# Kernel optimization log

Hardware: AMD Instinct MI355X
Metric: run time of the kernel (lower is better)

The kernel has to match this reference:

```python
import jax, jax.numpy as jnp
import numpy as np

B, S, E, H = 4, 1024, 1024, 16
D = E // H          # head_dim = 64
F = 4 * E           # mlp inner = 4096
EPS = 1e-5


def _layernorm(x, scale, bias):
    mu = jnp.mean(x, axis=-1, keepdims=True)
    var = jnp.var(x, axis=-1, keepdims=True)
    return (x - mu) * jax.lax.rsqrt(var + EPS) * scale + bias


def setup_inputs() -> dict:
    key = jax.random.key(0)
    ks = jax.random.split(key, 8)
    std = 0.02
    return {
        "hidden_states": jax.random.normal(ks[0], (B, S, E), jnp.float32),
        "ln1_scale": jnp.ones((E,), jnp.float32),
        "ln1_bias": jnp.zeros((E,), jnp.float32),
        # Conv1D kernels stored as (out_features, in_features), applied as x @ k.T
        "w_attn": jax.random.normal(ks[1], (3 * E, E), jnp.float32) * std,
        "b_attn": jnp.zeros((3 * E,), jnp.float32),
        "w_proj": jax.random.normal(ks[2], (E, E), jnp.float32) * std,
        "b_proj": jnp.zeros((E,), jnp.float32),
        "ln2_scale": jnp.ones((E,), jnp.float32),
        "ln2_bias": jnp.zeros((E,), jnp.float32),
        "w_fc": jax.random.normal(ks[3], (F, E), jnp.float32) * std,
        "b_fc": jnp.zeros((F,), jnp.float32),
        "w_proj2": jax.random.normal(ks[4], (E, F), jnp.float32) * std,
        "b_proj2": jnp.zeros((E,), jnp.float32),
    }


def reference(hidden_states, ln1_scale, ln1_bias, w_attn, b_attn, w_proj, b_proj,
              ln2_scale, ln2_bias, w_fc, b_fc, w_proj2, b_proj2):
    x = hidden_states
    # --- attention sub-block ---
    h = _layernorm(x, ln1_scale, ln1_bias)
    qkv = h @ w_attn.T + b_attn                      # [B,S,3E]
    q, k, v = jnp.split(qkv, 3, axis=2)
    q = q.reshape(B, S, H, D) / jnp.sqrt(jnp.float32(D))
    k = k.reshape(B, S, H, D)
    v = v.reshape(B, S, H, D)
    # NOTE: source sets attention_bias = None, so NO causal mask is applied.
    logits = jnp.einsum("bqhd,bkhd->bhqk", q, k)     # [B,H,S,S]
    attn = jax.nn.softmax(logits, axis=-1)
    o = jnp.einsum("bhqk,bkhd->bqhd", attn, v).reshape(B, S, E)
    o = o @ w_proj.T + b_proj
    x = x + o
    # --- mlp sub-block ---
    h = _layernorm(x, ln2_scale, ln2_bias)
    m = jax.nn.gelu(h @ w_fc.T + b_fc, approximate=True)  # gelu_new
    m = m @ w_proj2.T + b_proj2
    return x + m
```

## Files before the change

kernel.cpp:

```cpp
#include <hip/hip_runtime.h>

#define DEV __device__ __forceinline__

using bf16x8 = __attribute__((ext_vector_type(8))) __bf16;
using f32x4  = __attribute__((ext_vector_type(4))) float;
typedef unsigned int u32;
typedef unsigned short u16;
typedef unsigned long long u64;

static constexpr int Bb = 4, Ss = 1024, Ee = 1024, Hh = 16, Dd = 64, Ff = 4096;
static constexpr int Mm = Bb * Ss;

DEV u16 f2bf(float f) {
  union { float f; u32 u; } v; v.f = f;
  u32 r = v.u + 0x7fffu + ((v.u >> 16) & 1u);
  return (u16)(r >> 16);
}

DEV void gload16(const void* g, void* lds) {
  __builtin_amdgcn_global_load_lds(
      (const __attribute__((address_space(1))) void*)(u64)g,
      (__attribute__((address_space(3))) void*)(u32)(u64)lds,
      16, 0, 0);
}

DEV float gelu_tanh(float x) {
  float x3 = x * x * x;
  float t  = tanhf(0.7978845608028654f * (x + 0.044715f * x3));
  return 0.5f * x * (1.0f + t);
}

DEV int swz(int row, int col) { return row * 64 + (col ^ ((row & 7) << 3)); }

__global__ __launch_bounds__(256) void cvt_bf16(const float* __restrict__ in,
                                                u16* __restrict__ out, int n) {
  int i = (blockIdx.x * 256 + threadIdx.x) * 8;
  if (i >= n) return;
  float4 a = *(const float4*)(in + i);
  float4 b = *(const float4*)(in + i + 4);
  uint4 o;
  o.x = (u32)f2bf(a.x) | ((u32)f2bf(a.y) << 16);
  o.y = (u32)f2bf(a.z) | ((u32)f2bf(a.w) << 16);
  o.z = (u32)f2bf(b.x) | ((u32)f2bf(b.y) << 16);
  o.w = (u32)f2bf(b.z) | ((u32)f2bf(b.w) << 16);
  *(uint4*)(out + i) = o;
}

__global__ __launch_bounds__(256) void ln_kernel(const float* __restrict__ x,
                                                 const float* __restrict__ scale,
                                                 const float* __restrict__ bias,
                                                 u16* __restrict__ h) {
  const int row = blockIdx.x, tid = threadIdx.x;
  const float4 v = ((const float4*)(x + (size_t)row * Ee))[tid];
  float s  = v.x + v.y + v.z + v.w;
  float ss = v.x * v.x + v.y * v.y + v.z * v.z + v.w * v.w;
  for (int m = 1; m < 64; m <<= 1) {
    s  += __shfl_xor(s, m, 64);
    ss += __shfl_xor(ss, m, 64);
  }
  __shared__ float red[8];
  const int w = tid >> 6, ln = tid & 63;
  if (ln == 0) { red[w * 2] = s; red[w * 2 + 1] = ss; }
  __syncthreads();
  s  = red[0] + red[2] + red[4] + red[6];
  ss = red[1] + red[3] + red[5] + red[7];
  const float mu   = s * (1.0f / Ee);
  const float var  = ss * (1.0f / Ee) - mu * mu;
  const float rstd = rsqrtf(var + 1e-5f);
  const float4 sc = ((const float4*)scale)[tid];
  const float4 bi = ((const float4*)bias)[tid];
  ushort4 o;
  o.x = f2bf((v.x - mu) * rstd * sc.x + bi.x);
  o.y = f2bf((v.y - mu) * rstd * sc.y + bi.y);
  o.z = f2bf((v.z - mu) * rstd * sc.z + bi.z);
  o.w = f2bf((v.w - mu) * rstd * sc.w + bi.w);
  ((ushort4*)(h + (size_t)row * Ee))[tid] = o;
}

template <int EPI>
__global__ __launch_bounds__(256, 3) void gemm2(
    const u16* __restrict__ A, const u16* __restrict__ Bw,
    const float* __restrict__ bias, const float* __restrict__ resid,
    float* __restrict__ outf, u16* __restrict__ outb,
    u16* __restrict__ q, u16* __restrict__ k, u16* __restrict__ v,
    int N, int K) {
  __shared__ u16 As[3][128 * 32];
  __shared__ u16 Bs[3][128 * 32];
  const int tid = threadIdx.x;
  const int w = tid >> 6, ln = tid & 63;
  const int lr = ln & 15, lg = ln >> 4;

  const int nwg = gridDim.x * gridDim.y;
  const int bid = blockIdx.y * gridDim.x + blockIdx.x;
  const int sid = (bid & 7) * (nwg >> 3) + (bid >> 3);
  const int bx = sid % gridDim.x, by = sid / gridDim.x;
  const int tm = by * 128, tn = bx * 128;
  const int wr = (w >> 1) * 64, wc = (w & 1) * 64;

  f32x4 zero4 = {0.f, 0.f, 0.f, 0.f};
  f32x4 acc[4][4];
#pragma unroll
  for (int i = 0; i < 4; ++i)
#pragma unroll
    for (int j = 0; j < 4; ++j) acc[i][j] = zero4;

  const int r0 = tid >> 2, sl = tid & 3;
  const int cs = (sl ^ (r0 & 3)) * 8;
  const u16* aP0 = A  + (size_t)(tm + r0) * K + cs;
  const u16* aP1 = A  + (size_t)(tm + 64 + r0) * K + cs;
  const u16* bP0 = Bw + (size_t)(tn + r0) * K + cs;
  const u16* bP1 = Bw + (size_t)(tn + 64 + r0) * K + cs;

  auto STAGE = [&](int buf, int k0) {
    gload16(aP0 + k0, &As[buf][tid * 8]);
    gload16(aP1 + k0, &As[buf][(256 + tid) * 8]);
    gload16(bP0 + k0, &Bs[buf][tid * 8]);
    gload16(bP1 + k0, &Bs[buf][(256 + tid) * 8]);
  };

  const int nt = K >> 5;
  STAGE(0, 0);
  STAGE(1, 32);
  asm volatile("s_waitcnt vmcnt(4)" ::: "memory");
  __builtin_amdgcn_s_barrier();
  __builtin_amdgcn_sched_barrier(0);

  for (int t = 0; t < nt; ++t) {
    const int cur = t % 3;
    const bool more = (t + 2) < nt;
    if (more) STAGE((t + 2) % 3, (t + 2) << 5);

    bf16x8 af[4], bb[4];
#pragma unroll
    for (int mi = 0; mi < 4; ++mi) {
      const int row = wr + mi * 16 + lr;
      af[mi] = *(const bf16x8*)&As[cur][row * 32 + ((lg ^ (row & 3)) << 3)];
    }
#pragma unroll
    for (int ni = 0; ni < 4; ++ni) {
      const int row = wc + ni * 16 + lr;
      bb[ni] = *(const bf16x8*)&Bs[cur][row * 32 + ((lg ^ (row & 3)) << 3)];
    }
    __builtin_amdgcn_s_setprio(1);
#pragma unroll
    for (int mi = 0; mi < 4; ++mi)
#pragma unroll
      for (int ni = 0; ni < 4; ++ni)
        acc[mi][ni] = __builtin_amdgcn_mfma_f32_16x16x32_bf16(
            af[mi], bb[ni], acc[mi][ni], 0, 0, 0);
    __builtin_amdgcn_s_setprio(0);
    __builtin_amdgcn_sched_barrier(0);
    if (more) asm volatile("s_waitcnt vmcnt(4)" ::: "memory");
    else      asm volatile("s_waitcnt vmcnt(0)" ::: "memory");
    __builtin_amdgcn_s_barrier();
    __builtin_amdgcn_sched_barrier(0);
  }

#pragma unroll
  for (int mi = 0; mi < 4; ++mi) {
#pragma unroll
    for (int ni = 0; ni < 4; ++ni) {
      const int gc = tn + wc + ni * 16 + lr;
#pragma unroll
      for (int j = 0; j < 4; ++j) {
        const int gr = tm + wr + mi * 16 + lg * 4 + j;
        float val = acc[mi][ni][j] + bias[gc];
        if constexpr (EPI == 0) {
          const int which = gc >> 10, hh = (gc >> 6) & 15, dd = gc & 63;
          const int bb2 = gr >> 10, ss2 = gr & 1023;
          const size_t dst = ((size_t)(bb2 * 16 + hh) * 1024 + ss2) * 64 + dd;
          if (which == 0)      q[dst] = f2bf(val * 0.125f);
          else if (which == 1) k[dst] = f2bf(val);
          else                 v[dst] = f2bf(val);
        } else if constexpr (EPI == 1) {
          const size_t idx = (size_t)gr * N + gc;
          outf[idx] = val + resid[idx];
        } else {
          outb[(size_t)gr * N + gc] = f2bf(gelu_tanh(val));
        }
      }
    }
  }
}

__global__ __launch_bounds__(256) void attn_kernel(const u16* __restrict__ qg,
                                                   const u16* __restrict__ kg,
                                                   const u16* __restrict__ vg,
                                                   u16* __restrict__ ao) {
  __shared__ u16 Qs[64 * 64], Ks[64 * 64], Vt[64 * 64], Ps[64 * 64];
  const int tid = threadIdx.x;
  const int w = tid >> 6, ln = tid & 63;
  const int lr = ln & 15, lg = ln >> 4;
  const int bh = blockIdx.y;
  const int q0 = blockIdx.x * 64;
  const size_t head = (size_t)bh * (Ss * Dd);

  {
    const u16* src = qg + head + (size_t)q0 * Dd;
#pragma unroll
    for (int i = 0; i < 2; ++i) {
      const int gi = i * 256 + tid, row = gi >> 3, g = gi & 7;
      *(uint4*)&Qs[row * 64 + ((g ^ (row & 7)) << 3)] = *(const uint4*)(src + gi * 8);
    }
  }

  f32x4 zero4 = {0.f, 0.f, 0.f, 0.f};
  f32x4 acc_o[4] = {zero4, zero4, zero4, zero4};
  float mrow[4] = {-1e30f, -1e30f, -1e30f, -1e30f};
  float lrow[4] = {0.f, 0.f, 0.f, 0.f};

  for (int kt = 0; kt < 16; ++kt) {
    __syncthreads();
    const u16* ksrc = kg + head + (size_t)kt * 64 * Dd;
    const u16* vsrc = vg + head + (size_t)kt * 64 * Dd;
#pragma unroll
    for (int i = 0; i < 2; ++i) {
      const int gi = i * 256 + tid, row = gi >> 3, g = gi & 7;
      *(uint4*)&Ks[row * 64 + ((g ^ (row & 7)) << 3)] = *(const uint4*)(ksrc + gi * 8);
    }
#pragma unroll
    for (int i = 0; i < 2; ++i) {
      const int kv = i * 32 + (tid >> 3), d0 = (tid & 7) * 8;
      uint4 dv = *(const uint4*)(vsrc + (size_t)kv * Dd + d0);
      const u16* pv = (const u16*)&dv;
#pragma unroll
      for (int j = 0; j < 8; ++j) {
        const int dd = d0 + j;
        Vt[dd * 64 + (((kv >> 3) ^ (dd & 7)) << 3) + (kv & 7)] = pv[j];
      }
    }
    __syncthreads();

    bf16x8 aq[2];
#pragma unroll
    for (int kk = 0; kk < 2; ++kk)
      aq[kk] = *(const bf16x8*)&Qs[swz(w * 16 + lr, kk * 32 + lg * 8)];
    f32x4 sa[4];
#pragma unroll
    for (int kf = 0; kf < 4; ++kf) {
      f32x4 s = zero4;
#pragma unroll
      for (int kk = 0; kk < 2; ++kk) {
        bf16x8 bk = *(const bf16x8*)&Ks[swz(kf * 16 + lr, kk * 32 + lg * 8)];
        s = __builtin_amdgcn_mfma_f32_16x16x32_bf16(aq[kk], bk, s, 0, 0, 0);
      }
      sa[kf] = s;
    }

#pragma unroll
    for (int j = 0; j < 4; ++j) {
      float mx = fmaxf(fmaxf(sa[0][j], sa[1][j]), fmaxf(sa[2][j], sa[3][j]));
      mx = fmaxf(mx, __shfl_xor(mx, 1, 64));
      mx = fmaxf(mx, __shfl_xor(mx, 2, 64));
      mx = fmaxf(mx, __shfl_xor(mx, 4, 64));
      mx = fmaxf(mx, __shfl_xor(mx, 8, 64));
      const float nm = fmaxf(mrow[j], mx);
      const float corr = __expf(mrow[j] - nm);
      mrow[j] = nm;
      float ssum = 0.f;
#pragma unroll
      for (int kf = 0; kf < 4; ++kf) {
        const float p = __expf(sa[kf][j] - nm);
        sa[kf][j] = p;
        ssum += p;
      }
      ssum += __shfl_xor(ssum, 1, 64);
      ssum += __shfl_xor(ssum, 2, 64);
      ssum += __shfl_xor(ssum, 4, 64);
      ssum += __shfl_xor(ssum, 8, 64);
      lrow[j] = lrow[j] * corr + ssum;
#pragma unroll
      for (int df = 0; df < 4; ++df) acc_o[df][j] *= corr;
    }

#pragma unroll
    for (int kf = 0; kf < 4; ++kf)
#pragma unroll
      for (int j = 0; j < 4; ++j)
        Ps[swz(w * 16 + lg * 4 + j, kf * 16 + lr)] = f2bf(sa[kf][j]);

    __syncthreads();

    bf16x8 ap[2];
#pragma unroll
    for (int kk = 0; kk < 2; ++kk)
      ap[kk] = *(const bf16x8*)&Ps[swz(w * 16 + lr, kk * 32 + lg * 8)];
#pragma unroll
    for (int df = 0; df < 4; ++df) {
#pragma unroll
      for (int kk = 0; kk < 2; ++kk) {
        bf16x8 bv = *(const bf16x8*)&Vt[swz(df * 16 + lr, kk * 32 + lg * 8)];
        acc_o[df] = __builtin_amdgcn_mfma_f32_16x16x32_bf16(ap[kk], bv, acc_o[df], 0, 0, 0);
      }
    }
  }

  const int b = bh >> 4, h = bh & 15;
#pragma unroll
  for (int df = 0; df < 4; ++df) {
#pragma unroll
    for (int j = 0; j < 4; ++j) {
      const int srow = q0 + w * 16 + lg * 4 + j;
      const int e = h * 64 + df * 16 + lr;
      ao[((size_t)b * Ss + srow) * Ee + e] = f2bf(acc_o[df][j] / lrow[j]);
    }
  }
}

extern "C" void kernel_launch(void* const* d_in, const int* in_sizes, int n_in,
                              void* d_out, int out_size, void* d_ws, size_t ws_size,
                              hipStream_t stream) {
  const float* x      = (const float*)d_in[0];
  const float* ln1_s  = (const float*)d_in[1];
  const float* ln1_b  = (const float*)d_in[2];
  const float* w_attn = (const float*)d_in[3];
  const float* b_attn = (const float*)d_in[4];
  const float* w_proj = (const float*)d_in[5];
  const float* b_proj = (const float*)d_in[6];
  const float* ln2_s  = (const float*)d_in[7];
  const float* ln2_b  = (const float*)d_in[8];
  const float* w_fc   = (const float*)d_in[9];
  const float* b_fc   = (const float*)d_in[10];
  const float* w_proj2= (const float*)d_in[11];
  const float* b_proj2= (const float*)d_in[12];
  float* out = (float*)d_out;

  char* base = (char*)d_ws;
  size_t off = 0;
  auto alloc = [&](size_t bytes) { char* p = base + off; off += bytes; return p; };
  u16* wA   = (u16*)alloc((size_t)3 * Ee * Ee * 2);
  u16* wP   = (u16*)alloc((size_t)Ee * Ee * 2);
  u16* wF   = (u16*)alloc((size_t)Ff * Ee * 2);
  u16* wP2  = (u16*)alloc((size_t)Ee * Ff * 2);
  u16* h1   = (u16*)alloc((size_t)Mm * Ee * 2);
  u16* qws  = (u16*)alloc((size_t)Mm * Ee * 2);
  u16* kws  = (u16*)alloc((size_t)Mm * Ee * 2);
  u16* vws  = (u16*)alloc((size_t)Mm * Ee * 2);
  u16* aws  = (u16*)alloc((size_t)Mm * Ee * 2);
  float* x1 = (float*)alloc((size_t)Mm * Ee * 4);
  u16* mfc  = qws;

  cvt_bf16<<<3 * Ee * Ee / 2048, 256, 0, stream>>>(w_attn, wA, 3 * Ee * Ee);
  cvt_bf16<<<Ee * Ee / 2048, 256, 0, stream>>>(w_proj, wP, Ee * Ee);
  cvt_bf16<<<Ff * Ee / 2048, 256, 0, stream>>>(w_fc, wF, Ff * Ee);
  cvt_bf16<<<Ee * Ff / 2048, 256, 0, stream>>>(w_proj2, wP2, Ee * Ff);

  ln_kernel<<<Mm, 256, 0, stream>>>(x, ln1_s, ln1_b, h1);
  gemm2<0><<<dim3(24, 32), 256, 0, stream>>>(h1, wA, b_attn, nullptr,
                                             nullptr, nullptr, qws, kws, vws,
                                             3 * Ee, Ee);
  attn_kernel<<<dim3(16, 64), 256, 0, stream>>>(qws, kws, vws, aws);
  gemm2<1><<<dim3(8, 32), 256, 0, stream>>>(aws, wP, b_proj, x,
                                            x1, nullptr, nullptr, nullptr, nullptr,
                                            Ee, Ee);
  ln_kernel<<<Mm, 256, 0, stream>>>(x1, ln2_s, ln2_b, h1);
  gemm2<2><<<dim3(32, 32), 256, 0, stream>>>(h1, wF, b_fc, nullptr,
                                             nullptr, mfc, nullptr, nullptr, nullptr,
                                             Ff, Ee);
  gemm2<1><<<dim3(8, 32), 256, 0, stream>>>(mfc, wP2, b_proj2, x1,
                                            out, nullptr, nullptr, nullptr, nullptr,
                                            Ee, Ff);
}
```

Measured before the change: 285.3 us.

## Add 256x256-tile 8-wave GEMM for QKV and FC projections

Introduces a new GEMM kernel with 256x256 output tiles, 512 threads (8 waves, each computing a 128x64 sub-tile), a K-step of 64 and double-buffered LDS fed by direct global-to-LDS loads. It interleaves LDS fragment reads with MFMA phases separated by barriers. The QKV and MLP-FC GEMMs switch to it to raise data reuse per tile and cut global/LDS traffic per flop. The cost is higher register and LDS pressure (two waves per SIMD target) and fewer workgroups: 192 for QKV and 256 for FC on a 256-CU part, which may leave tail imbalance.

```diff
diff --git a/kernel.cpp b/kernel.cpp
--- a/kernel.cpp
+++ b/kernel.cpp
@@ -31,6 +31,10 @@
 }
 
 DEV int swz(int row, int col) { return row * 64 + (col ^ ((row & 7) << 3)); }
+
+DEV f32x4 MFMA(bf16x8 a, bf16x8 b, f32x4 c) {
+  return __builtin_amdgcn_mfma_f32_16x16x32_bf16(a, b, c, 0, 0, 0);
+}
 
 __global__ __launch_bounds__(256) void cvt_bf16(const float* __restrict__ in,
                                                 u16* __restrict__ out, int n) {
@@ -78,6 +82,134 @@
 }
 
 template <int EPI>
+__global__ __launch_bounds__(512, 2) void gemm8p(
+    const u16* __restrict__ A, const u16* __restrict__ Bw,
+    const float* __restrict__ bias,
+    u16* __restrict__ outb,
+    u16* __restrict__ q, u16* __restrict__ k, u16* __restrict__ v,
+    int N, int K) {
+  __shared__ u16 As8[2][256 * 64];
+  __shared__ u16 Bs8[2][256 * 64];
+  const int tid = threadIdx.x;
+  const int w = tid >> 6, ln = tid & 63;
+  const int lr = ln & 15, lg = ln >> 4;
+  const int wr = w >> 2, wc = w & 3;
+
+  const int nwg = gridDim.x * gridDim.y;
+  const int bid = blockIdx.y * gridDim.x + blockIdx.x;
+  const int sid = (bid & 7) * (nwg >> 3) + (bid >> 3);
+  const int bx = sid % gridDim.x, by = sid / gridDim.x;
+  const int tm = by * 256, tn = bx * 256;
+
+  f32x4 acc[8][4];
+  f32x4 zero4 = {0.f, 0.f, 0.f, 0.f};
+#pragma unroll
+  for (int i = 0; i < 8; ++i)
+#pragma unroll
+    for (int j = 0; j < 4; ++j) acc[i][j] = zero4;
+
+  const int rA = tid >> 3;
+  const int slv = (tid & 7) ^ (rA & 7);
+  const u16* aS = A  + (size_t)(tm + rA) * K + (slv << 3);
+  const u16* bS = Bw + (size_t)(tn + rA) * K + (slv << 3);
+  const size_t g64 = (size_t)64 * K;
+
+  auto STAGE = [&](int t) {
+    const int c = t & 1;
+    const int kc = t << 6;
+#pragma unroll
+    for (int g = 0; g < 4; ++g)
+      gload16(aS + (size_t)g * g64 + kc, &As8[c][g * 4096 + tid * 8]);
+#pragma unroll
+    for (int g = 0; g < 4; ++g)
+      gload16(bS + (size_t)g * g64 + kc, &Bs8[c][g * 4096 + tid * 8]);
+  };
+
+  const int sk0 = ((lg) ^ (lr & 7)) << 3;
+  const int sk1 = ((4 | lg) ^ (lr & 7)) << 3;
+  const int aBase = (wr * 128 + lr) * 64;
+  const int bBase = (wc * 64 + lr) * 64;
+
+  const int nkt = K >> 6;
+  STAGE(0);
+  STAGE(1);
+  asm volatile("s_waitcnt vmcnt(8)" ::: "memory");
+  __builtin_amdgcn_s_barrier();
+  __builtin_amdgcn_sched_barrier(0);
+
+  for (int kt = 0; kt < nkt; ++kt) {
+    const u16* Ab = &As8[kt & 1][0];
+    const u16* Bbuf = &Bs8[kt & 1][0];
+    bf16x8 bfr[4][2];
+#pragma unroll
+    for (int ph = 0; ph < 4; ++ph) {
+      if (ph == 0) {
+#pragma unroll
+        for (int n = 0; n < 4; ++n) {
+          bfr[n][0] = *(const bf16x8*)&Bbuf[bBase + n * 1024 + sk0];
+          bfr[n][1] = *(const bf16x8*)&Bbuf[bBase + n * 1024 + sk1];
+        }
+      }
+      bf16x8 a00 = *(const bf16x8*)&Ab[aBase + (2 * ph) * 1024 + sk0];
+      bf16x8 a01 = *(const bf16x8*)&Ab[aBase + (2 * ph) * 1024 + sk1];
+      bf16x8 a10 = *(const bf16x8*)&Ab[aBase + (2 * ph + 1) * 1024 + sk0];
+      bf16x8 a11 = *(const bf16x8*)&Ab[aBase + (2 * ph + 1) * 1024 + sk1];
+      __builtin_amdgcn_sched_barrier(0);
+      __builtin_amdgcn_s_barrier();
+      __builtin_amdgcn_sched_barrier(0);
+      __builtin_amdgcn_s_setprio(1);
+#pragma unroll
+      for (int n = 0; n < 4; ++n) {
+        acc[2 * ph][n]     = MFMA(a00, bfr[n][0], acc[2 * ph][n]);
+        acc[2 * ph + 1][n] = MFMA(a10, bfr[n][0], acc[2 * ph + 1][n]);
+      }
+#pragma unroll
+      for (int n = 0; n < 4; ++n) {
+        acc[2 * ph][n]     = MFMA(a01, bfr[n][1], acc[2 * ph][n]);
+        acc[2 * ph + 1][n] = MFMA(a11, bfr[n][1], acc[2 * ph + 1][n]);
+      }
+      __builtin_amdgcn_s_setprio(0);
+      __builtin_amdgcn_sched_barrier(0);
+      __builtin_amdgcn_s_barrier();
+    }
+    if (kt + 2 < nkt) {
+      __builtin_amdgcn_sched_barrier(0);
+      STAGE(kt + 2);
+      asm volatile("s_waitcnt vmcnt(8)" ::: "memory");
+    } else if (kt + 1 < nkt) {
+      asm volatile("s_waitcnt vmcnt(0)" ::: "memory");
+    }
+    if (kt + 1 < nkt) {
+      __builtin_amdgcn_s_barrier();
+      __builtin_amdgcn_sched_barrier(0);
+    }
+  }
+
+#pragma unroll
+  for (int mi = 0; mi < 8; ++mi) {
+#pragma unroll
+    for (int ni = 0; ni < 4; ++ni) {
+      const int gc = tn + wc * 64 + ni * 16 + lr;
+#pragma unroll
+      for (int j = 0; j < 4; ++j) {
+        const int gr = tm + wr * 128 + mi * 16 + lg * 4 + j;
+        float val = acc[mi][ni][j] + bias[gc];
+        if constexpr (EPI == 0) {
+          const int which = gc >> 10, hh = (gc >> 6) & 15, dd = gc & 63;
+          const int bb2 = gr >> 10, ss2 = gr & 1023;
+          const size_t dst = ((size_t)(bb2 * 16 + hh) * 1024 + ss2) * 64 + dd;
+          if (which == 0)      q[dst] = f2bf(val * 0.125f);
+          else if (which == 1) k[dst] = f2bf(val);
+          else                 v[dst] = f2bf(val);
+        } else {
+          outb[(size_t)gr * N + gc] = f2bf(gelu_tanh(val));
+        }
+      }
+    }
+  }
+}
+
+template <int EPI>
 __global__ __launch_bounds__(256, 3) void gemm2(
     const u16* __restrict__ A, const u16* __restrict__ Bw,
     const float* __restrict__ bias, const float* __restrict__ resid,
@@ -146,8 +278,7 @@
     for (int mi = 0; mi < 4; ++mi)
 #pragma unroll
       for (int ni = 0; ni < 4; ++ni)
-        acc[mi][ni] = __builtin_amdgcn_mfma_f32_16x16x32_bf16(
-            af[mi], bb[ni], acc[mi][ni], 0, 0, 0);
+        acc[mi][ni] = MFMA(af[mi], bb[ni], acc[mi][ni]);
     __builtin_amdgcn_s_setprio(0);
     __builtin_amdgcn_sched_barrier(0);
     if (more) asm volatile("s_waitcnt vmcnt(4)" ::: "memory");
@@ -165,14 +296,7 @@
       for (int j = 0; j < 4; ++j) {
         const int gr = tm + wr + mi * 16 + lg * 4 + j;
         float val = acc[mi][ni][j] + bias[gc];
-        if constexpr (EPI == 0) {
-          const int which = gc >> 10, hh = (gc >> 6) & 15, dd = gc & 63;
-          const int bb2 = gr >> 10, ss2 = gr & 1023;
-          const size_t dst = ((size_t)(bb2 * 16 + hh) * 1024 + ss2) * 64 + dd;
-          if (which == 0)      q[dst] = f2bf(val * 0.125f);
-          else if (which == 1) k[dst] = f2bf(val);
-          else                 v[dst] = f2bf(val);
-        } else if constexpr (EPI == 1) {
+        if constexpr (EPI == 1) {
           const size_t idx = (size_t)gr * N + gc;
           outf[idx] = val + resid[idx];
         } else {
@@ -242,7 +366,7 @@
 #pragma unroll
       for (int kk = 0; kk < 2; ++kk) {
         bf16x8 bk = *(const bf16x8*)&Ks[swz(kf * 16 + lr, kk * 32 + lg * 8)];
-        s = __builtin_amdgcn_mfma_f32_16x16x32_bf16(aq[kk], bk, s, 0, 0, 0);
+        s = MFMA(aq[kk], bk, s);
       }
       sa[kf] = s;
     }
@@ -290,7 +414,7 @@
 #pragma unroll
       for (int kk = 0; kk < 2; ++kk) {
         bf16x8 bv = *(const bf16x8*)&Vt[swz(df * 16 + lr, kk * 32 + lg * 8)];
-        acc_o[df] = __builtin_amdgcn_mfma_f32_16x16x32_bf16(ap[kk], bv, acc_o[df], 0, 0, 0);
+        acc_o[df] = MFMA(ap[kk], bv, acc_o[df]);
       }
     }
   }
@@ -346,17 +470,17 @@
   cvt_bf16<<<Ee * Ff / 2048, 256, 0, stream>>>(w_proj2, wP2, Ee * Ff);
 
   ln_kernel<<<Mm, 256, 0, stream>>>(x, ln1_s, ln1_b, h1);
-  gemm2<0><<<dim3(24, 32), 256, 0, stream>>>(h1, wA, b_attn, nullptr,
-                                             nullptr, nullptr, qws, kws, vws,
-                                             3 * Ee, Ee);
+  gemm8p<0><<<dim3(12, 16), 512, 0, stream>>>(h1, wA, b_attn,
+                                              nullptr, qws, kws, vws,
+                                              3 * Ee, Ee);
   attn_kernel<<<dim3(16, 64), 256, 0, stream>>>(qws, kws, vws, aws);
   gemm2<1><<<dim3(8, 32), 256, 0, stream>>>(aws, wP, b_proj, x,
                                             x1, nullptr, nullptr, nullptr, nullptr,
                                             Ee, Ee);
   ln_kernel<<<Mm, 256, 0, stream>>>(x1, ln2_s, ln2_b, h1);
-  gemm2<2><<<dim3(32, 32), 256, 0, stream>>>(h1, wF, b_fc, nullptr,
-                                             nullptr, mfc, nullptr, nullptr, nullptr,
-                                             Ff, Ee);
+  gemm8p<2><<<dim3(16, 16), 512, 0, stream>>>(h1, wF, b_fc,
+                                              mfc, nullptr, nullptr, nullptr,
+                                              Ff, Ee);
   gemm2<1><<<dim3(8, 32), 256, 0, stream>>>(mfc, wP2, b_proj2, x1,
                                             out, nullptr, nullptr, nullptr, nullptr,
                                             Ee, Ff);
```

After: 329.2 us. 15.4% more time.

## Template GEMM on per-warp tile shape, shrink tiles and use double buffering

Applied to the files above, without the earlier changes.

Replaces the fixed 128x128 triple-buffered GEMM with a templated gemm3 whose block tile is AM*32 x AN*32. It uses 128x64 tiles for the QKV and FC GEMMs and 64x64 tiles for the two output projections, which raises the grid size. Shared-memory buffering drops from three stages to two, with a full vmcnt(0) wait every iteration. The setprio and sched_barrier hints are removed, and launch bounds now request 5 blocks per CU. More blocks and occupancy could help the small N=1024 projections, but smaller tiles lower reuse per load and the shallower prefetch exposes more global-load latency.

```diff
diff --git a/kernel.cpp b/kernel.cpp
--- a/kernel.cpp
+++ b/kernel.cpp
@@ -31,6 +31,10 @@
 }
 
 DEV int swz(int row, int col) { return row * 64 + (col ^ ((row & 7) << 3)); }
+
+DEV f32x4 MFMA(bf16x8 a, bf16x8 b, f32x4 c) {
+  return __builtin_amdgcn_mfma_f32_16x16x32_bf16(a, b, c, 0, 0, 0);
+}
 
 __global__ __launch_bounds__(256) void cvt_bf16(const float* __restrict__ in,
                                                 u16* __restrict__ out, int n) {
@@ -77,93 +81,87 @@
   ((ushort4*)(h + (size_t)row * Ee))[tid] = o;
 }
 
-template <int EPI>
-__global__ __launch_bounds__(256, 3) void gemm2(
+template <int EPI, int AM, int AN>
+__global__ __launch_bounds__(256, 5) void gemm3(
     const u16* __restrict__ A, const u16* __restrict__ Bw,
     const float* __restrict__ bias, const float* __restrict__ resid,
     float* __restrict__ outf, u16* __restrict__ outb,
     u16* __restrict__ q, u16* __restrict__ k, u16* __restrict__ v,
     int N, int K) {
-  __shared__ u16 As[3][128 * 32];
-  __shared__ u16 Bs[3][128 * 32];
+  constexpr int BM = AM * 32, BN = AN * 32;
+  constexpr int GA = BM / 64, GB = BN / 64;
+  __shared__ u16 As[2][BM * 32];
+  __shared__ u16 Bs[2][BN * 32];
   const int tid = threadIdx.x;
   const int w = tid >> 6, ln = tid & 63;
   const int lr = ln & 15, lg = ln >> 4;
+  const int wr = w >> 1, wc = w & 1;
 
   const int nwg = gridDim.x * gridDim.y;
   const int bid = blockIdx.y * gridDim.x + blockIdx.x;
   const int sid = (bid & 7) * (nwg >> 3) + (bid >> 3);
   const int bx = sid % gridDim.x, by = sid / gridDim.x;
-  const int tm = by * 128, tn = bx * 128;
-  const int wr = (w >> 1) * 64, wc = (w & 1) * 64;
-
+  const int tm = by * BM, tn = bx * BN;
+
+  f32x4 acc[AM][AN];
   f32x4 zero4 = {0.f, 0.f, 0.f, 0.f};
-  f32x4 acc[4][4];
-#pragma unroll
-  for (int i = 0; i < 4; ++i)
-#pragma unroll
-    for (int j = 0; j < 4; ++j) acc[i][j] = zero4;
-
-  const int r0 = tid >> 2, sl = tid & 3;
-  const int cs = (sl ^ (r0 & 3)) * 8;
-  const u16* aP0 = A  + (size_t)(tm + r0) * K + cs;
-  const u16* aP1 = A  + (size_t)(tm + 64 + r0) * K + cs;
-  const u16* bP0 = Bw + (size_t)(tn + r0) * K + cs;
-  const u16* bP1 = Bw + (size_t)(tn + 64 + r0) * K + cs;
+#pragma unroll
+  for (int i = 0; i < AM; ++i)
+#pragma unroll
+    for (int j = 0; j < AN; ++j) acc[i][j] = zero4;
+
+  const int r0 = tid >> 2;
+  const int cs = ((tid & 3) ^ (r0 & 3)) * 8;
+  const u16* aP[GA];
+  const u16* bP[GB];
+#pragma unroll
+  for (int i = 0; i < GA; ++i) aP[i] = A + (size_t)(tm + r0 + i * 64) * K + cs;
+#pragma unroll
+  for (int i = 0; i < GB; ++i) bP[i] = Bw + (size_t)(tn + r0 + i * 64) * K + cs;
 
   auto STAGE = [&](int buf, int k0) {
-    gload16(aP0 + k0, &As[buf][tid * 8]);
-    gload16(aP1 + k0, &As[buf][(256 + tid) * 8]);
-    gload16(bP0 + k0, &Bs[buf][tid * 8]);
-    gload16(bP1 + k0, &Bs[buf][(256 + tid) * 8]);
+#pragma unroll
+    for (int i = 0; i < GA; ++i)
+      gload16(aP[i] + k0, &As[buf][(tid + i * 256) * 8]);
+#pragma unroll
+    for (int i = 0; i < GB; ++i)
+      gload16(bP[i] + k0, &Bs[buf][(tid + i * 256) * 8]);
   };
 
+  const int fsl = (lg ^ (lr & 3)) << 3;
   const int nt = K >> 5;
   STAGE(0, 0);
-  STAGE(1, 32);
-  asm volatile("s_waitcnt vmcnt(4)" ::: "memory");
+  asm volatile("s_waitcnt vmcnt(0)" ::: "memory");
   __builtin_amdgcn_s_barrier();
-  __builtin_amdgcn_sched_barrier(0);
 
   for (int t = 0; t < nt; ++t) {
-    const int cur = t % 3;
-    const bool more = (t + 2) < nt;
-    if (more) STAGE((t + 2) % 3, (t + 2) << 5);
-
-    bf16x8 af[4], bb[4];
-#pragma unroll
-    for (int mi = 0; mi < 4; ++mi) {
-      const int row = wr + mi * 16 + lr;
-      af[mi] = *(const bf16x8*)&As[cur][row * 32 + ((lg ^ (row & 3)) << 3)];
-    }
-#pragma unroll
-    for (int ni = 0; ni < 4; ++ni) {
-      const int row = wc + ni * 16 + lr;
-      bb[ni] = *(const bf16x8*)&Bs[cur][row * 32 + ((lg ^ (row & 3)) << 3)];
-    }
-    __builtin_amdgcn_s_setprio(1);
-#pragma unroll
-    for (int mi = 0; mi < 4; ++mi)
-#pragma unroll
-      for (int ni = 0; ni < 4; ++ni)
-        acc[mi][ni] = __builtin_amdgcn_mfma_f32_16x16x32_bf16(
-            af[mi], bb[ni], acc[mi][ni], 0, 0, 0);
-    __builtin_amdgcn_s_setprio(0);
-    __builtin_amdgcn_sched_barrier(0);
-    if (more) asm volatile("s_waitcnt vmcnt(4)" ::: "memory");
-    else      asm volatile("s_waitcnt vmcnt(0)" ::: "memory");
+    if (t + 1 < nt) STAGE((t + 1) & 1, (t + 1) << 5);
+    const u16* Ab = &As[t & 1][0];
+    const u16* Bbuf = &Bs[t & 1][0];
+    bf16x8 af[AM], bf[AN];
+#pragma unroll
+    for (int mi = 0; mi < AM; ++mi)
+      af[mi] = *(const bf16x8*)&Ab[(wr * AM * 16 + mi * 16 + lr) * 32 + fsl];
+#pragma unroll
+    for (int ni = 0; ni < AN; ++ni)
+      bf[ni] = *(const bf16x8*)&Bbuf[(wc * AN * 16 + ni * 16 + lr) * 32 + fsl];
+#pragma unroll
+    for (int mi = 0; mi < AM; ++mi)
+#pragma unroll
+      for (int ni = 0; ni < AN; ++ni)
+        acc[mi][ni] = MFMA(af[mi], bf[ni], acc[mi][ni]);
+    asm volatile("s_waitcnt vmcnt(0)" ::: "memory");
     __builtin_amdgcn_s_barrier();
-    __builtin_amdgcn_sched_barrier(0);
-  }
-
-#pragma unroll
-  for (int mi = 0; mi < 4; ++mi) {
-#pragma unroll
-    for (int ni = 0; ni < 4; ++ni) {
-      const int gc = tn + wc + ni * 16 + lr;
+  }
+
+#pragma unroll
+  for (int mi = 0; mi < AM; ++mi) {
+#pragma unroll
+    for (int ni = 0; ni < AN; ++ni) {
+      const int gc = tn + wc * AN * 16 + ni * 16 + lr;
 #pragma unroll
       for (int j = 0; j < 4; ++j) {
-        const int gr = tm + wr + mi * 16 + lg * 4 + j;
+        const int gr = tm + wr * AM * 16 + mi * 16 + lg * 4 + j;
         float val = acc[mi][ni][j] + bias[gc];
         if constexpr (EPI == 0) {
           const int which = gc >> 10, hh = (gc >> 6) & 15, dd = gc & 63;
@@ -242,7 +240,7 @@
 #pragma unroll
       for (int kk = 0; kk < 2; ++kk) {
         bf16x8 bk = *(const bf16x8*)&Ks[swz(kf * 16 + lr, kk * 32 + lg * 8)];
-        s = __builtin_amdgcn_mfma_f32_16x16x32_bf16(aq[kk], bk, s, 0, 0, 0);
+        s = MFMA(aq[kk], bk, s);
       }
       sa[kf] = s;
     }
@@ -290,7 +288,7 @@
 #pragma unroll
       for (int kk = 0; kk < 2; ++kk) {
         bf16x8 bv = *(const bf16x8*)&Vt[swz(df * 16 + lr, kk * 32 + lg * 8)];
-        acc_o[df] = __builtin_amdgcn_mfma_f32_16x16x32_bf16(ap[kk], bv, acc_o[df], 0, 0, 0);
+        acc_o[df] = MFMA(ap[kk], bv, acc_o[df]);
       }
     }
   }
@@ -346,18 +344,18 @@
   cvt_bf16<<<Ee * Ff / 2048, 256, 0, stream>>>(w_proj2, wP2, Ee * Ff);
 
   ln_kernel<<<Mm, 256, 0, stream>>>(x, ln1_s, ln1_b, h1);
-  gemm2<0><<<dim3(24, 32), 256, 0, stream>>>(h1, wA, b_attn, nullptr,
-                                             nullptr, nullptr, qws, kws, vws,
-                                             3 * Ee, Ee);
+  gemm3<0, 4, 2><<<dim3(48, 32), 256, 0, stream>>>(h1, wA, b_attn, nullptr,
+                                                   nullptr, nullptr, qws, kws, vws,
+                                                   3 * Ee, Ee);
   attn_kernel<<<dim3(16, 64), 256, 0, stream>>>(qws, kws, vws, aws);
-  gemm2<1><<<dim3(8, 32), 256, 0, stream>>>(aws, wP, b_proj, x,
-                                            x1, nullptr, nullptr, nullptr, nullptr,
-                                            Ee, Ee);
+  gemm3<1, 2, 2><<<dim3(16, 64), 256, 0, stream>>>(aws, wP, b_proj, x,
+                                                   x1, nullptr, nullptr, nullptr, nullptr,
+                                                   Ee, Ee);
   ln_kernel<<<Mm, 256, 0, stream>>>(x1, ln2_s, ln2_b, h1);
-  gemm2<2><<<dim3(32, 32), 256, 0, stream>>>(h1, wF, b_fc, nullptr,
-                                             nullptr, mfc, nullptr, nullptr, nullptr,
-                                             Ff, Ee);
-  gemm2<1><<<dim3(8, 32), 256, 0, stream>>>(mfc, wP2, b_proj2, x1,
-                                            out, nullptr, nullptr, nullptr, nullptr,
-                                            Ee, Ff);
-}
+  gemm3<2, 4, 2><<<dim3(64, 32), 256, 0, stream>>>(h1, wF, b_fc, nullptr,
+                                                   nullptr, mfc, nullptr, nullptr, nullptr,
+                                                   Ff, Ee);
+  gemm3<1, 2, 2><<<dim3(16, 64), 256, 0, stream>>>(mfc, wP2, b_proj2, x1,
+                                                   out, nullptr, nullptr, nullptr, nullptr,
+                                                   Ee, Ff);
+}
```

New measurement: 307.1 us. 7.6% more time.
